# Kernel optimization log

Measured on AMD Instinct MI355X. Metric: run time of the kernel, lower is better.

Reference implementation:

```python
import jax, jax.numpy as jnp
import numpy as np

B, T, F, H, NH, L = 32, 512, 16, 64, 4, 2
HD = H // NH


def _ln(x, g, b, eps=1e-5):
    m = x.mean(-1, keepdims=True)
    v = ((x - m) ** 2).mean(-1, keepdims=True)
    return (x - m) / jnp.sqrt(v + eps) * g + b


def _glu(x, w, b):
    a, g = jnp.split(x @ w + b, 2, axis=-1)
    return a * jax.nn.sigmoid(g)


def _lstm_layer(x, w_ih, w_hh, b):
    # x: (B,T,H); PyTorch gate order i,f,g,o
    Bd = x.shape[0]

    def step(carry, xt):
        h, c = carry
        gates = xt @ w_ih + h @ w_hh + b
        i, f, g, o = jnp.split(gates, 4, axis=-1)
        c = jax.nn.sigmoid(f) * c + jax.nn.sigmoid(i) * jnp.tanh(g)
        h = jax.nn.sigmoid(o) * jnp.tanh(c)
        return (h, c), h

    z = jnp.zeros((Bd, H), x.dtype)
    _, hs = jax.lax.scan(step, (z, z), jnp.swapaxes(x, 0, 1))
    return jnp.swapaxes(hs, 0, 1)


def setup_inputs() -> dict:
    key = jax.random.key(0)
    specs = [
        ("x", (B, T, F), "n"),
        ("ip_w", (H,), "n"), ("ip_b", (H,), "n"),
        ("vsn_fc1_w", (F, H, H), "n"), ("vsn_fc1_b", (F, H), "n"),
        ("vsn_fc2_w", (F, H, 2 * H), "n"), ("vsn_fc2_b", (F, 2 * H), "n"),
        ("vsn_ln_g", (F, H), "1"), ("vsn_ln_b", (F, H), "0"),
        ("sel_fc1_w", (F * H, H), "n"), ("sel_fc1_b", (H,), "n"),
        ("sel_fc2_w", (H, 2 * F), "n"), ("sel_fc2_b", (2 * F,), "n"),
        ("sel_skip_w", (F * H, F), "n"), ("sel_skip_b", (F,), "n"),
        ("sel_ln_g", (F,), "1"), ("sel_ln_b", (F,), "0"),
        ("lstm_w_ih", (L, H, 4 * H), "n"), ("lstm_w_hh", (L, H, 4 * H), "n"), ("lstm_b", (L, 4 * H), "n"),
        ("plg_w", (H, 2 * H), "n"), ("plg_b", (2 * H,), "n"),
        ("pln_g", (H,), "1"), ("pln_b", (H,), "0"),
        ("qkv_w", (H, 3 * H), "n"), ("qkv_b", (3 * H,), "n"),
        ("ao_w", (H, H), "n"), ("ao_b", (H,), "n"),
        ("pag_w", (H, 2 * H), "n"), ("pag_b", (2 * H,), "n"),
        ("pan_g", (H,), "1"), ("pan_b", (H,), "0"),
        ("ff1_w", (H, 4 * H), "n"), ("ff1_b", (4 * H,), "n"),
        ("ff2_w", (4 * H, 2 * H), "n"), ("ff2_b", (2 * H,), "n"),
        ("ffln_g", (H,), "1"), ("ffln_b", (H,), "0"),
        ("fn_g", (H,), "1"), ("fn_b", (H,), "0"),
        ("out_w", (H, 1), "n"), ("out_b", (1,), "n"),
    ]
    keys = jax.random.split(key, len(specs))
    d = {}
    for (name, shp, kind), k in zip(specs, keys):
        if kind == "n":
            scale = 1.0 if name == "x" else 0.05
            d[name] = jax.random.normal(k, shp, jnp.float32) * scale
        elif kind == "1":
            d[name] = jnp.ones(shp, jnp.float32)
        else:
            d[name] = jnp.zeros(shp, jnp.float32)
    return d


def reference(x, ip_w, ip_b, vsn_fc1_w, vsn_fc1_b, vsn_fc2_w, vsn_fc2_b, vsn_ln_g, vsn_ln_b,
              sel_fc1_w, sel_fc1_b, sel_fc2_w, sel_fc2_b, sel_skip_w, sel_skip_b, sel_ln_g, sel_ln_b,
              lstm_w_ih, lstm_w_hh, lstm_b, plg_w, plg_b, pln_g, pln_b,
              qkv_w, qkv_b, ao_w, ao_b, pag_w, pag_b, pan_g, pan_b,
              ff1_w, ff1_b, ff2_w, ff2_b, ffln_g, ffln_b, fn_g, fn_b, out_w, out_b):
    Bd, Td, Fd = x.shape
    # input_proj: Linear(1,H) applied to each scalar feature -> (B,T,F,H)
    xp = x[..., None] * ip_w + ip_b
    # --- VSN (vectorized over B and T; torch loops over T and F) ---
    flat = xp.reshape(Bd, Td, Fd * H)
    h = jax.nn.elu(flat @ sel_fc1_w + sel_fc1_b)
    a, g = jnp.split(h @ sel_fc2_w + sel_fc2_b, 2, axis=-1)
    sel = _ln(a * jax.nn.sigmoid(g) + (flat @ sel_skip_w + sel_skip_b), sel_ln_g, sel_ln_b)
    w = jax.nn.softmax(sel, axis=-1)  # (B,T,F)
    h = jax.nn.elu(jnp.einsum('btfi,fio->btfo', xp, vsn_fc1_w) + vsn_fc1_b)
    a, g = jnp.split(jnp.einsum('btfi,fio->btfo', h, vsn_fc2_w) + vsn_fc2_b, 2, axis=-1)
    proc = _ln(a * jax.nn.sigmoid(g) + xp, vsn_ln_g, vsn_ln_b)  # (B,T,F,H)
    vsn_out = jnp.einsum('btf,btfh->bth', w, proc)
    # --- 2-layer LSTM encoder (dropout inactive in eval) ---
    seq = vsn_out
    for l in range(L):
        seq = _lstm_layer(seq, lstm_w_ih[l], lstm_w_hh[l], lstm_b[l])
    lo = _ln(_glu(seq, plg_w, plg_b) + vsn_out, pln_g, pln_b)
    # --- self-attention ---
    q, k, v = jnp.split(lo @ qkv_w + qkv_b, 3, axis=-1)
    q = q.reshape(Bd, Td, NH, HD)
    k = k.reshape(Bd, Td, NH, HD)
    v = v.reshape(Bd, Td, NH, HD)
    sc = jnp.einsum('bqhd,bkhd->bhqk', q, k) / jnp.sqrt(jnp.float32(HD))
    att = jnp.einsum('bhqk,bkhd->bqhd', jax.nn.softmax(sc, axis=-1), v).reshape(Bd, Td, H)
    att = att @ ao_w + ao_b
    at = _ln(_glu(att, pag_w, pag_b) + lo, pan_g, pan_b)
    # --- FF GRN + final norm ---
    h = jax.nn.elu(at @ ff1_w + ff1_b)
    a, g = jnp.split(h @ ff2_w + ff2_b, 2, axis=-1)
    ff = _ln(a * jax.nn.sigmoid(g) + at, ffln_g, ffln_b)
    ff = _ln(ff + at, fn_g, fn_b)
    return ff[:, -1, :] @ out_w + out_b  # (B, forecast_horizon)
```

## Files before the change

kernel.cpp:

```cpp
#include <hip/hip_runtime.h>
#include <math.h>


__device__ __forceinline__ float sigf(float x){
    return 1.f / (1.f + __expf(-x));
}
__device__ __forceinline__ float tanhf_(float x){
    float xc = fminf(fmaxf(x, -15.f), 15.f);
    float e = __expf(-2.f * xc);
    return (1.f - e) / (1.f + e);
}
__device__ __forceinline__ float eluf(float x){
    return x > 0.f ? x : (__expf(x) - 1.f);
}
__device__ __forceinline__ float wsum64(float v){
    #pragma unroll
    for (int o = 1; o < 64; o <<= 1) v += __shfl_xor(v, o, 64);
    return v;
}
__device__ __forceinline__ float wmax64(float v){
    #pragma unroll
    for (int o = 1; o < 64; o <<= 1) v = fmaxf(v, __shfl_xor(v, o, 64));
    return v;
}

#define BARRIER_LGKM() do {                                    \
    asm volatile("s_waitcnt lgkmcnt(0)" ::: "memory");         \
    __builtin_amdgcn_s_barrier();                              \
} while(0)

__global__ __launch_bounds__(256) void tft_vsn_kernel(
    const float* __restrict__ x,
    const float* __restrict__ ip_w, const float* __restrict__ ip_b,
    const float* __restrict__ vfc1w, const float* __restrict__ vfc1b,
    const float* __restrict__ vfc2w, const float* __restrict__ vfc2b,
    const float* __restrict__ vlng, const float* __restrict__ vlnb,
    const float* __restrict__ sfc1w, const float* __restrict__ sfc1b,
    const float* __restrict__ sfc2w, const float* __restrict__ sfc2b,
    const float* __restrict__ sskw, const float* __restrict__ sskb,
    const float* __restrict__ slng, const float* __restrict__ slnb,
    float* __restrict__ vsn_out)
{
    __shared__ __align__(16) float s_x[512];
    __shared__ __align__(16) float s_ipw[64];
    __shared__ __align__(16) float s_ipb[64];
    __shared__ __align__(16) float s_xp[32*65];
    __shared__ __align__(16) float s_W1[64*64];
    __shared__ __align__(16) float s_W2[64*128];
    __shared__ __align__(16) float s_Wsk[64*16];
    __shared__ __align__(16) float s_h[32*65];
    __shared__ __align__(16) float s_sel2[32*32];
    __shared__ __align__(16) float s_wsm[32*16];
    __shared__ __align__(16) float s_lng[64];
    __shared__ __align__(16) float s_lnb[64];
    __shared__ __align__(16) float s_b1[64];
    __shared__ __align__(16) float s_b2[128];

    const int tid  = threadIdx.x;
    const int pos0 = blockIdx.x * 32;
    const int m    = tid >> 3;
    const int g8   = tid & 7;
    const int j0   = g8 * 8;

    if (tid < 128) ((float4*)s_x)[tid] = *(const float4*)(x + pos0*16 + tid*4);
    if (tid < 64) { s_ipw[tid] = ip_w[tid]; s_ipb[tid] = ip_b[tid]; }
    __syncthreads();

    float accS[8];
    #pragma unroll
    for (int i = 0; i < 8; i++) accS[i] = 0.f;
    float accK0 = 0.f, accK1 = 0.f;

    for (int f = 0; f < 16; f++){
        {
            float xb = s_x[m*16 + f];
            #pragma unroll
            for (int i = 0; i < 8; i++)
                s_xp[m*65 + j0 + i] = xb * s_ipw[j0+i] + s_ipb[j0+i];
        }
        #pragma unroll
        for (int i = 0; i < 4; i++)
            ((float4*)s_W1)[tid + i*256] = *(const float4*)(sfc1w + f*4096 + (tid + i*256)*4);
        ((float4*)s_Wsk)[tid] = *(const float4*)(sskw + f*1024 + tid*4);
        __syncthreads();
        #pragma unroll 8
        for (int k = 0; k < 64; k++){
            float xv = s_xp[m*65 + k];
            const float4* wr = (const float4*)(s_W1 + k*64 + j0);
            float4 w0 = wr[0], w1 = wr[1];
            accS[0] += xv*w0.x; accS[1] += xv*w0.y; accS[2] += xv*w0.z; accS[3] += xv*w0.w;
            accS[4] += xv*w1.x; accS[5] += xv*w1.y; accS[6] += xv*w1.z; accS[7] += xv*w1.w;
            float2 wk = *(const float2*)(s_Wsk + k*16 + g8*2);
            accK0 += xv*wk.x; accK1 += xv*wk.y;
        }
        __syncthreads();
    }

    #pragma unroll
    for (int i = 0; i < 8; i++)
        s_h[m*65 + j0 + i] = eluf(accS[i] + sfc1b[j0+i]);
    ((float4*)s_W1)[tid]       = *(const float4*)(sfc2w + tid*4);
    ((float4*)s_W1)[tid + 256] = *(const float4*)(sfc2w + 1024 + tid*4);
    __syncthreads();

    {
        const int jj = g8 * 4;
        float a0 = 0.f, a1 = 0.f, a2 = 0.f, a3 = 0.f;
        #pragma unroll 8
        for (int k = 0; k < 64; k++){
            float hv = s_h[m*65 + k];
            float4 w = *(const float4*)(s_W1 + k*32 + jj);
            a0 += hv*w.x; a1 += hv*w.y; a2 += hv*w.z; a3 += hv*w.w;
        }
        s_sel2[m*32 + jj+0] = a0 + sfc2b[jj+0];
        s_sel2[m*32 + jj+1] = a1 + sfc2b[jj+1];
        s_sel2[m*32 + jj+2] = a2 + sfc2b[jj+2];
        s_sel2[m*32 + jj+3] = a3 + sfc2b[jj+3];
    }
    __syncthreads();

    {
        const int f0 = g8 * 2;
        float a0 = s_sel2[m*32 + f0],   g0 = s_sel2[m*32 + 16 + f0];
        float a1 = s_sel2[m*32 + f0+1], g1 = s_sel2[m*32 + 16 + f0+1];
        float pre0 = a0*sigf(g0) + accK0 + sskb[f0];
        float pre1 = a1*sigf(g1) + accK1 + sskb[f0+1];
        float sum = pre0 + pre1;
        sum += __shfl_xor(sum,1,8); sum += __shfl_xor(sum,2,8); sum += __shfl_xor(sum,4,8);
        float mean = sum * 0.0625f;
        float d0 = pre0 - mean, d1 = pre1 - mean;
        float vv = d0*d0 + d1*d1;
        vv += __shfl_xor(vv,1,8); vv += __shfl_xor(vv,2,8); vv += __shfl_xor(vv,4,8);
        float rstd = rsqrtf(vv * 0.0625f + 1e-5f);
        float sv0 = d0*rstd*slng[f0]   + slnb[f0];
        float sv1 = d1*rstd*slng[f0+1] + slnb[f0+1];
        float mx = fmaxf(sv0, sv1);
        mx = fmaxf(mx, __shfl_xor(mx,1,8));
        mx = fmaxf(mx, __shfl_xor(mx,2,8));
        mx = fmaxf(mx, __shfl_xor(mx,4,8));
        float e0 = __expf(sv0 - mx), e1 = __expf(sv1 - mx);
        float es = e0 + e1;
        es += __shfl_xor(es,1,8); es += __shfl_xor(es,2,8); es += __shfl_xor(es,4,8);
        float inv = 1.f / es;
        s_wsm[m*16 + f0]   = e0 * inv;
        s_wsm[m*16 + f0+1] = e1 * inv;
    }
    __syncthreads();

    float accV[8];
    #pragma unroll
    for (int i = 0; i < 8; i++) accV[i] = 0.f;

    for (int f = 0; f < 16; f++){
        {
            float xb = s_x[m*16 + f];
            #pragma unroll
            for (int i = 0; i < 8; i++)
                s_xp[m*65 + j0 + i] = xb * s_ipw[j0+i] + s_ipb[j0+i];
        }
        #pragma unroll
        for (int i = 0; i < 4; i++)
            ((float4*)s_W1)[tid + i*256] = *(const float4*)(vfc1w + f*4096 + (tid + i*256)*4);
        #pragma unroll
        for (int i = 0; i < 8; i++)
            ((float4*)s_W2)[tid + i*256] = *(const float4*)(vfc2w + f*8192 + (tid + i*256)*4);
        if (tid < 16)       ((float4*)s_b1)[tid]     = *(const float4*)(vfc1b + f*64  + tid*4);
        else if (tid < 48)  ((float4*)s_b2)[tid-16]  = *(const float4*)(vfc2b + f*128 + (tid-16)*4);
        else if (tid < 64)  ((float4*)s_lng)[tid-48] = *(const float4*)(vlng  + f*64  + (tid-48)*4);
        else if (tid < 80)  ((float4*)s_lnb)[tid-64] = *(const float4*)(vlnb  + f*64  + (tid-64)*4);
        __syncthreads();

        float ah[8];
        #pragma unroll
        for (int i = 0; i < 8; i++) ah[i] = 0.f;
        #pragma unroll 8
        for (int k = 0; k < 64; k++){
            float xv = s_xp[m*65 + k];
            const float4* wr = (const float4*)(s_W1 + k*64 + j0);
            float4 w0 = wr[0], w1 = wr[1];
            ah[0] += xv*w0.x; ah[1] += xv*w0.y; ah[2] += xv*w0.z; ah[3] += xv*w0.w;
            ah[4] += xv*w1.x; ah[5] += xv*w1.y; ah[6] += xv*w1.z; ah[7] += xv*w1.w;
        }
        #pragma unroll
        for (int i = 0; i < 8; i++)
            s_h[m*65 + j0 + i] = eluf(ah[i] + s_b1[j0+i]);
        __syncthreads();

        float aa[8], ag[8];
        #pragma unroll
        for (int i = 0; i < 8; i++){ aa[i] = 0.f; ag[i] = 0.f; }
        #pragma unroll 4
        for (int k = 0; k < 64; k++){
            float hv = s_h[m*65 + k];
            const float4* war = (const float4*)(s_W2 + k*128 + j0);
            const float4* wgr = (const float4*)(s_W2 + k*128 + 64 + j0);
            float4 wa0 = war[0], wa1 = war[1];
            float4 wg0 = wgr[0], wg1 = wgr[1];
            aa[0] += hv*wa0.x; aa[1] += hv*wa0.y; aa[2] += hv*wa0.z; aa[3] += hv*wa0.w;
            aa[4] += hv*wa1.x; aa[5] += hv*wa1.y; aa[6] += hv*wa1.z; aa[7] += hv*wa1.w;
            ag[0] += hv*wg0.x; ag[1] += hv*wg0.y; ag[2] += hv*wg0.z; ag[3] += hv*wg0.w;
            ag[4] += hv*wg1.x; ag[5] += hv*wg1.y; ag[6] += hv*wg1.z; ag[7] += hv*wg1.w;
        }
        float pre[8];
        float lsum = 0.f;
        #pragma unroll
        for (int i = 0; i < 8; i++){
            float av = aa[i] + s_b2[j0+i];
            float gv = ag[i] + s_b2[64 + j0+i];
            pre[i] = av * sigf(gv) + s_xp[m*65 + j0 + i];
            lsum += pre[i];
        }
        lsum += __shfl_xor(lsum,1,8); lsum += __shfl_xor(lsum,2,8); lsum += __shfl_xor(lsum,4,8);
        float mean = lsum * 0.015625f;
        float lvar = 0.f;
        #pragma unroll
        for (int i = 0; i < 8; i++){ float d = pre[i] - mean; lvar += d*d; }
        lvar += __shfl_xor(lvar,1,8); lvar += __shfl_xor(lvar,2,8); lvar += __shfl_xor(lvar,4,8);
        float rstd = rsqrtf(lvar * 0.015625f + 1e-5f);
        float wf = s_wsm[m*16 + f];
        #pragma unroll
        for (int i = 0; i < 8; i++)
            accV[i] += wf * ((pre[i] - mean) * rstd * s_lng[j0+i] + s_lnb[j0+i]);
        __syncthreads();
    }

    float4 o0 = make_float4(accV[0], accV[1], accV[2], accV[3]);
    float4 o1 = make_float4(accV[4], accV[5], accV[6], accV[7]);
    *(float4*)(vsn_out + (pos0 + m)*64 + j0)     = o0;
    *(float4*)(vsn_out + (pos0 + m)*64 + j0 + 4) = o1;
}

__global__ __launch_bounds__(256) void tft_xgates_kernel(
    const float* __restrict__ vsn, const float* __restrict__ w_ih,
    const float* __restrict__ bias, float* __restrict__ gpre)
{
    __shared__ __align__(16) float s_w[64*256];
    __shared__ __align__(16) float s_vT[64*20];
    __shared__ __align__(16) float s_b[256];
    const int tid  = threadIdx.x;
    const int pos0 = blockIdx.x * 16;

    #pragma unroll
    for (int i = 0; i < 16; i++)
        ((float4*)s_w)[tid + i*256] = *(const float4*)(w_ih + (tid + i*256)*4);
    s_b[tid] = bias[tid];
    {
        int mm = tid >> 4;
        int k0 = (tid & 15) * 4;
        float4 v = *(const float4*)(vsn + (pos0 + mm)*64 + k0);
        s_vT[(k0+0)*20 + mm] = v.x;
        s_vT[(k0+1)*20 + mm] = v.y;
        s_vT[(k0+2)*20 + mm] = v.z;
        s_vT[(k0+3)*20 + mm] = v.w;
    }
    __syncthreads();

    float acc[16];
    #pragma unroll
    for (int i = 0; i < 16; i++) acc[i] = 0.f;
    #pragma unroll 8
    for (int k = 0; k < 64; k++){
        float wv = s_w[k*256 + tid];
        const float4* vr = (const float4*)(s_vT + k*20);
        float4 v0 = vr[0], v1 = vr[1], v2 = vr[2], v3 = vr[3];
        acc[0]  += wv*v0.x; acc[1]  += wv*v0.y; acc[2]  += wv*v0.z; acc[3]  += wv*v0.w;
        acc[4]  += wv*v1.x; acc[5]  += wv*v1.y; acc[6]  += wv*v1.z; acc[7]  += wv*v1.w;
        acc[8]  += wv*v2.x; acc[9]  += wv*v2.y; acc[10] += wv*v2.z; acc[11] += wv*v2.w;
        acc[12] += wv*v3.x; acc[13] += wv*v3.y; acc[14] += wv*v3.z; acc[15] += wv*v3.w;
    }
    float bv = s_b[tid];
    #pragma unroll
    for (int i = 0; i < 16; i++)
        gpre[(pos0 + i)*256 + tid] = acc[i] + bv;
}

#define LDW4(P, i) make_float4((P)[(4*(i)+0)*256], (P)[(4*(i)+1)*256], \
                               (P)[(4*(i)+2)*256], (P)[(4*(i)+3)*256])

#define LSTM_CH(c) {                                                        \
    float4 h1c = h1b[c];                                                    \
    a10 += h1c.x*W1_##c.x; a11 += h1c.y*W1_##c.y;                           \
    a12 += h1c.z*W1_##c.z; a13 += h1c.w*W1_##c.w;                           \
    a20 += h1c.x*WX_##c.x; a21 += h1c.y*WX_##c.y;                           \
    a22 += h1c.z*WX_##c.z; a23 += h1c.w*WX_##c.w;                           \
    float4 h2c = h2b[c];                                                    \
    a20 += h2c.x*WH_##c.x; a21 += h2c.y*WH_##c.y;                           \
    a22 += h2c.z*WH_##c.z; a23 += h2c.w*WH_##c.w;                           \
}

__global__ __launch_bounds__(512, 1) void tft_lstm_kernel(
    const float* __restrict__ w_ih, const float* __restrict__ w_hh,
    const float* __restrict__ bias, const float* __restrict__ gpre,
    float* __restrict__ seq)
{
    __shared__ __align__(16) float s_h1[64];
    __shared__ __align__(16) float s_h2[64];
    __shared__ __align__(16) float s_g1h[512];
    __shared__ __align__(16) float s_g2h[512];
    __shared__ __align__(16) float s_gp[256];

    const int tid  = threadIdx.x;
    const int b    = blockIdx.x;
    const int g    = tid & 255;
    const int half = tid >> 8;
    const int koff = half * 32;

    const float* p1 = w_hh + koff*256 + g;
    const float* px = w_ih + 16384 + koff*256 + g;
    const float* ph = w_hh + 16384 + koff*256 + g;

    float4 W1_0 = LDW4(p1,0), W1_1 = LDW4(p1,1), W1_2 = LDW4(p1,2), W1_3 = LDW4(p1,3);
    float4 W1_4 = LDW4(p1,4), W1_5 = LDW4(p1,5), W1_6 = LDW4(p1,6), W1_7 = LDW4(p1,7);
    float4 WX_0 = LDW4(px,0), WX_1 = LDW4(px,1), WX_2 = LDW4(px,2), WX_3 = LDW4(px,3);
    float4 WX_4 = LDW4(px,4), WX_5 = LDW4(px,5), WX_6 = LDW4(px,6), WX_7 = LDW4(px,7);
    float4 WH_0 = LDW4(ph,0), WH_1 = LDW4(ph,1), WH_2 = LDW4(ph,2), WH_3 = LDW4(ph,3);
    float4 WH_4 = LDW4(ph,4), WH_5 = LDW4(ph,5), WH_6 = LDW4(ph,6), WH_7 = LDW4(ph,7);

    const float b2 = (half == 0) ? bias[256 + g] : 0.f;

    if (tid < 64) s_h1[tid] = 0.f;
    else if (tid < 128) s_h2[tid - 64] = 0.f;

    const float* gpb = gpre + (size_t)b * 512 * 256 + g;
    float gp_w = 0.f, gp_l = 0.f;
    if (half == 0){
        s_gp[g] = gpb[0];
        gp_w    = gpb[256];
        gp_l    = gpb[512];
    }
    float c1 = 0.f, c2 = 0.f;
    __syncthreads();

    const float4* h1b = (const float4*)s_h1 + half*8;
    const float4* h2b = (const float4*)s_h2 + half*8;
    float* seqb = seq + (size_t)b * 512 * 64;

    for (int n = 0; n <= 512; ++n){
        float a10 = (half == 0) ? s_gp[g] : 0.f;
        float a11 = 0.f, a12 = 0.f, a13 = 0.f;
        float a20 = b2, a21 = 0.f, a22 = 0.f, a23 = 0.f;
        LSTM_CH(0) LSTM_CH(1) LSTM_CH(2) LSTM_CH(3)
        LSTM_CH(4) LSTM_CH(5) LSTM_CH(6) LSTM_CH(7)
        float gp_n = 0.f;
        if (half == 0 && n + 3 < 512) gp_n = gpb[(n + 3) * 256];
        s_g1h[half*256 + g] = (a10 + a11) + (a12 + a13);
        s_g2h[half*256 + g] = (a20 + a21) + (a22 + a23);
        BARRIER_LGKM();

        if (tid < 64 && n < 512){
            float gi = s_g1h[tid]     + s_g1h[256+tid];
            float gf = s_g1h[64+tid]  + s_g1h[320+tid];
            float gg = s_g1h[128+tid] + s_g1h[384+tid];
            float go = s_g1h[192+tid] + s_g1h[448+tid];
            c1 = sigf(gf)*c1 + sigf(gi)*tanhf_(gg);
            s_h1[tid] = sigf(go)*tanhf_(c1);
        } else if (tid >= 64 && tid < 128 && n >= 1){
            int j = tid - 64;
            float gi = s_g2h[j]     + s_g2h[256+j];
            float gf = s_g2h[64+j]  + s_g2h[320+j];
            float gg = s_g2h[128+j] + s_g2h[384+j];
            float go = s_g2h[192+j] + s_g2h[448+j];
            c2 = sigf(gf)*c2 + sigf(gi)*tanhf_(gg);
            float h2v = sigf(go)*tanhf_(c2);
            s_h2[j] = h2v;
            seqb[(size_t)(n - 1)*64 + j] = h2v;
        }
        if (half == 0 && n + 1 < 512) s_gp[g] = gp_w;
        gp_w = gp_l; gp_l = gp_n;
        BARRIER_LGKM();
    }
}

__global__ __launch_bounds__(256) void tft_lokv_kernel(
    const float* __restrict__ seq, const float* __restrict__ vsn,
    const float* __restrict__ plgw, const float* __restrict__ plgb,
    const float* __restrict__ png,  const float* __restrict__ pnb,
    const float* __restrict__ qkvw, const float* __restrict__ qkvb,
    float* __restrict__ kbuf, float* __restrict__ vbuf,
    float* __restrict__ qlast, float* __restrict__ lolast)
{
    __shared__ __align__(16) float s_pw[64*128];
    __shared__ __align__(16) float s_qw[64*192];
    __shared__ __align__(16) float s_pb[128];
    __shared__ __align__(16) float s_png[64];
    __shared__ __align__(16) float s_pnb[64];
    __shared__ __align__(16) float s_qb[192];
    __shared__ __align__(16) float s_row[4][64];
    __shared__ __align__(16) float s_lo[4][64];

    const int tid  = threadIdx.x;
    const int lane = tid & 63;
    const int wid  = tid >> 6;

    #pragma unroll
    for (int i = 0; i < 8; i++)
        ((float4*)s_pw)[tid + i*256] = *(const float4*)(plgw + (tid + i*256)*4);
    #pragma unroll
    for (int i = 0; i < 12; i++)
        ((float4*)s_qw)[tid + i*256] = *(const float4*)(qkvw + (tid + i*256)*4);
    if (tid < 128) s_pb[tid] = plgb[tid];
    if (tid < 64){ s_png[tid] = png[tid]; s_pnb[tid] = pnb[tid]; }
    if (tid < 192) s_qb[tid] = qkvb[tid];
    __syncthreads();

    for (int it = 0; it < 16; it++){
        int mpos = blockIdx.x*64 + wid*16 + it;
        int b = mpos >> 9, t = mpos & 511;
        float sv = seq[mpos*64 + lane];
        float vs = vsn[mpos*64 + lane];
        s_row[wid][lane] = sv;
        __syncthreads();
        float a = s_pb[lane], g = s_pb[64 + lane];
        #pragma unroll 8
        for (int k = 0; k < 64; k++){
            float rv = s_row[wid][k];
            a += rv * s_pw[k*128 + lane];
            g += rv * s_pw[k*128 + 64 + lane];
        }
        float pre = a * sigf(g) + vs;
        float mean = wsum64(pre) * 0.015625f;
        float d = pre - mean;
        float vv = wsum64(d*d) * 0.015625f;
        float lo = d * rsqrtf(vv + 1e-5f) * s_png[lane] + s_pnb[lane];
        s_lo[wid][lane] = lo;
        __syncthreads();
        float ka = s_qb[64 + lane], va = s_qb[128 + lane];
        #pragma unroll 8
        for (int k = 0; k < 64; k++){
            float lv = s_lo[wid][k];
            ka += lv * s_qw[k*192 + 64 + lane];
            va += lv * s_qw[k*192 + 128 + lane];
        }
        int h = lane >> 4, dd = lane & 15;
        kbuf[((b*4 + h)*512 + t)*16 + dd] = ka;
        vbuf[((b*4 + h)*512 + t)*16 + dd] = va;
        if (t == 511){
            float qa = s_qb[lane];
            #pragma unroll 8
            for (int k = 0; k < 64; k++)
                qa += s_lo[wid][k] * s_qw[k*192 + lane];
            qlast[b*64 + lane] = qa;
            lolast[b*64 + lane] = lo;
        }
    }
}

__global__ __launch_bounds__(256) void tft_head_kernel(
    const float* __restrict__ kbuf, const float* __restrict__ vbuf,
    const float* __restrict__ qlast, const float* __restrict__ lolast,
    const float* __restrict__ aow,  const float* __restrict__ aob,
    const float* __restrict__ pagw, const float* __restrict__ pagb,
    const float* __restrict__ pang, const float* __restrict__ panb,
    const float* __restrict__ ff1w, const float* __restrict__ ff1b,
    const float* __restrict__ ff2w, const float* __restrict__ ff2b,
    const float* __restrict__ fflng, const float* __restrict__ fflnb,
    const float* __restrict__ fng,  const float* __restrict__ fnb,
    const float* __restrict__ outw, const float* __restrict__ outb,
    float* __restrict__ out)
{
    __shared__ __align__(16) float s_q[64];
    __shared__ __align__(16) float s_lo[64];
    __shared__ __align__(16) float s_sc[4*512];
    __shared__ __align__(16) float s_part[4][64];
    __shared__ __align__(16) float s_a[64];
    __shared__ __align__(16) float s_a2[64];
    __shared__ __align__(16) float s_z[128];
    __shared__ __align__(16) float s_at[64];
    __shared__ __align__(16) float s_f1[256];

    const int tid = threadIdx.x;
    const int b   = blockIdx.x;
    if (tid < 64){ s_q[tid] = qlast[b*64 + tid]; s_lo[tid] = lolast[b*64 + tid]; }
    __syncthreads();

    for (int idx = tid; idx < 2048; idx += 256){
        int h = idx >> 9, t = idx & 511;
        const float4* kr = (const float4*)(kbuf + ((b*4 + h)*512 + t)*16);
        const float4* qr = (const float4*)(s_q + h*16);
        float4 k0 = kr[0], k1 = kr[1], k2 = kr[2], k3 = kr[3];
        float4 q0 = qr[0], q1 = qr[1], q2 = qr[2], q3 = qr[3];
        float d = q0.x*k0.x + q0.y*k0.y + q0.z*k0.z + q0.w*k0.w
                + q1.x*k1.x + q1.y*k1.y + q1.z*k1.z + q1.w*k1.w
                + q2.x*k2.x + q2.y*k2.y + q2.z*k2.z + q2.w*k2.w
                + q3.x*k3.x + q3.y*k3.y + q3.z*k3.z + q3.w*k3.w;
        s_sc[idx] = d * 0.25f;
    }
    __syncthreads();
    {
        int h = tid >> 6, lane = tid & 63;
        float v[8];
        float mx = -1e30f;
        #pragma unroll
        for (int j = 0; j < 8; j++){ v[j] = s_sc[h*512 + lane + j*64]; mx = fmaxf(mx, v[j]); }
        mx = wmax64(mx);
        float sum = 0.f;
        #pragma unroll
        for (int j = 0; j < 8; j++){ v[j] = __expf(v[j] - mx); sum += v[j]; }
        sum = wsum64(sum);
        float inv = 1.f / sum;
        #pragma unroll
        for (int j = 0; j < 8; j++) s_sc[h*512 + lane + j*64] = v[j] * inv;
    }
    __syncthreads();
    {
        int j = tid & 63, part = tid >> 6;
        int h = j >> 4, dd = j & 15;
        float pa = 0.f;
        for (int t = part*128; t < (part+1)*128; t++)
            pa += s_sc[h*512 + t] * vbuf[((b*4 + h)*512 + t)*16 + dd];
        s_part[part][j] = pa;
    }
    __syncthreads();
    if (tid < 64) s_a[tid] = s_part[0][tid] + s_part[1][tid] + s_part[2][tid] + s_part[3][tid];
    __syncthreads();
    if (tid < 64){
        float o = aob[tid];
        #pragma unroll 8
        for (int k = 0; k < 64; k++) o += s_a[k] * aow[k*64 + tid];
        s_a2[tid] = o;
    }
    __syncthreads();
    if (tid < 128){
        float z = pagb[tid];
        #pragma unroll 8
        for (int k = 0; k < 64; k++) z += s_a2[k] * pagw[k*128 + tid];
        s_z[tid] = z;
    }
    __syncthreads();
    if (tid < 64){
        float pre = s_z[tid] * sigf(s_z[64 + tid]) + s_lo[tid];
        float mean = wsum64(pre) * 0.015625f;
        float d = pre - mean;
        float vv = wsum64(d*d) * 0.015625f;
        s_at[tid] = d * rsqrtf(vv + 1e-5f) * pang[tid] + panb[tid];
    }
    __syncthreads();
    {
        float hv = ff1b[tid];
        #pragma unroll 8
        for (int k = 0; k < 64; k++) hv += s_at[k] * ff1w[k*256 + tid];
        s_f1[tid] = eluf(hv);
    }
    __syncthreads();
    if (tid < 128){
        float z = ff2b[tid];
        #pragma unroll 8
        for (int k = 0; k < 256; k++) z += s_f1[k] * ff2w[k*128 + tid];
        s_z[tid] = z;
    }
    __syncthreads();
    if (tid < 64){
        float pre = s_z[tid] * sigf(s_z[64 + tid]) + s_at[tid];
        float mean = wsum64(pre) * 0.015625f;
        float d = pre - mean;
        float vv = wsum64(d*d) * 0.015625f;
        float ffv = d * rsqrtf(vv + 1e-5f) * fflng[tid] + fflnb[tid];
        float pre2 = ffv + s_at[tid];
        float mean2 = wsum64(pre2) * 0.015625f;
        float d2 = pre2 - mean2;
        float v2 = wsum64(d2*d2) * 0.015625f;
        float f2 = d2 * rsqrtf(v2 + 1e-5f) * fng[tid] + fnb[tid];
        float p = wsum64(f2 * outw[tid]);
        if (tid == 0) out[b] = p + outb[0];
    }
}

extern "C" void kernel_launch(void* const* d_in, const int* in_sizes, int n_in,
                              void* d_out, int out_size, void* d_ws, size_t ws_size,
                              hipStream_t stream)
{
    const float* x     = (const float*)d_in[0];
    const float* ip_w  = (const float*)d_in[1];
    const float* ip_b  = (const float*)d_in[2];
    const float* vfc1w = (const float*)d_in[3];
    const float* vfc1b = (const float*)d_in[4];
    const float* vfc2w = (const float*)d_in[5];
    const float* vfc2b = (const float*)d_in[6];
    const float* vlng  = (const float*)d_in[7];
    const float* vlnb  = (const float*)d_in[8];
    const float* sfc1w = (const float*)d_in[9];
    const float* sfc1b = (const float*)d_in[10];
    const float* sfc2w = (const float*)d_in[11];
    const float* sfc2b = (const float*)d_in[12];
    const float* sskw  = (const float*)d_in[13];
    const float* sskb  = (const float*)d_in[14];
    const float* slng  = (const float*)d_in[15];
    const float* slnb  = (const float*)d_in[16];
    const float* lwih  = (const float*)d_in[17];
    const float* lwhh  = (const float*)d_in[18];
    const float* lb    = (const float*)d_in[19];
    const float* plgw  = (const float*)d_in[20];
    const float* plgb  = (const float*)d_in[21];
    const float* plng  = (const float*)d_in[22];
    const float* plnb  = (const float*)d_in[23];
    const float* qkvw  = (const float*)d_in[24];
    const float* qkvb  = (const float*)d_in[25];
    const float* aow   = (const float*)d_in[26];
    const float* aob   = (const float*)d_in[27];
    const float* pagw  = (const float*)d_in[28];
    const float* pagb  = (const float*)d_in[29];
    const float* pang  = (const float*)d_in[30];
    const float* panb  = (const float*)d_in[31];
    const float* ff1w  = (const float*)d_in[32];
    const float* ff1b  = (const float*)d_in[33];
    const float* ff2w  = (const float*)d_in[34];
    const float* ff2b  = (const float*)d_in[35];
    const float* fflng = (const float*)d_in[36];
    const float* fflnb = (const float*)d_in[37];
    const float* fng   = (const float*)d_in[38];
    const float* fnb   = (const float*)d_in[39];
    const float* outw  = (const float*)d_in[40];
    const float* outb  = (const float*)d_in[41];

    float* ws      = (float*)d_ws;
    float* vsn_out = ws;
    float* seq     = ws + 1048576;
    float* gpre    = ws + 2*1048576;
    float* kbuf    = ws + 6*1048576;
    float* vbuf    = ws + 7*1048576;
    float* qlast   = ws + 8*1048576;
    float* lolast  = qlast + 2048;
    float* outp    = (float*)d_out;

    tft_vsn_kernel<<<512, 256, 0, stream>>>(x, ip_w, ip_b, vfc1w, vfc1b, vfc2w, vfc2b,
                                            vlng, vlnb, sfc1w, sfc1b, sfc2w, sfc2b,
                                            sskw, sskb, slng, slnb, vsn_out);
    tft_xgates_kernel<<<1024, 256, 0, stream>>>(vsn_out, lwih, lb, gpre);
    tft_lstm_kernel<<<32, 512, 0, stream>>>(lwih, lwhh, lb, gpre, seq);
    tft_lokv_kernel<<<256, 256, 0, stream>>>(seq, vsn_out, plgw, plgb, plng, plnb,
                                             qkvw, qkvb, kbuf, vbuf, qlast, lolast);
    tft_head_kernel<<<32, 256, 0, stream>>>(kbuf, vbuf, qlast, lolast, aow, aob,
                                            pagw, pagb, pang, panb, ff1w, ff1b,
                                            ff2w, ff2b, fflng, fflnb, fng, fnb,
                                            outw, outb, outp);
}
```

Measured before the change: 767.9 us.

## Restructure LSTM recurrence to reduce gates in-wave and use one barrier per step

Reorganizes the persistent 2-layer LSTM kernel so each wave owns 16 hidden units. Lanes split the K dimension and gate pairs, and gate partial sums are combined with cross-lane shuffles instead of being staged in shared memory. Hidden states are double-buffered, which removes one of the two block barriers per timestep and the serial 64-thread gate phase. The cost is more weight registers for layer-2 waves (which take the full K=128 concat) and redundant activation math across lanes.

```diff
diff --git a/kernel.cpp b/kernel.cpp
--- a/kernel.cpp
+++ b/kernel.cpp
@@ -274,100 +274,133 @@
         gpre[(pos0 + i)*256 + tid] = acc[i] + bv;
 }
 
-#define LDW4(P, i) make_float4((P)[(4*(i)+0)*256], (P)[(4*(i)+1)*256], \
-                               (P)[(4*(i)+2)*256], (P)[(4*(i)+3)*256])
-
-#define LSTM_CH(c) {                                                        \
-    float4 h1c = h1b[c];                                                    \
-    a10 += h1c.x*W1_##c.x; a11 += h1c.y*W1_##c.y;                           \
-    a12 += h1c.z*W1_##c.z; a13 += h1c.w*W1_##c.w;                           \
-    a20 += h1c.x*WX_##c.x; a21 += h1c.y*WX_##c.y;                           \
-    a22 += h1c.z*WX_##c.z; a23 += h1c.w*WX_##c.w;                           \
-    float4 h2c = h2b[c];                                                    \
-    a20 += h2c.x*WH_##c.x; a21 += h2c.y*WH_##c.y;                           \
-    a22 += h2c.z*WH_##c.z; a23 += h2c.w*WH_##c.w;                           \
-}
+#define LW(P, c) make_float4((P)[(4*(c)+0)*256], (P)[(4*(c)+1)*256], \
+                             (P)[(4*(c)+2)*256], (P)[(4*(c)+3)*256])
+
+#define ACC(c, hv) { float4 h_ = (hv);                                      \
+    a0  += h_.x*WA_##c.x; a0x += h_.y*WA_##c.y;                             \
+    a0  += h_.z*WA_##c.z; a0x += h_.w*WA_##c.w;                             \
+    a1  += h_.x*WB_##c.x; a1x += h_.y*WB_##c.y;                             \
+    a1  += h_.z*WB_##c.z; a1x += h_.w*WB_##c.w; }
 
 __global__ __launch_bounds__(512, 1) void tft_lstm_kernel(
     const float* __restrict__ w_ih, const float* __restrict__ w_hh,
     const float* __restrict__ bias, const float* __restrict__ gpre,
     float* __restrict__ seq)
 {
-    __shared__ __align__(16) float s_h1[64];
-    __shared__ __align__(16) float s_h2[64];
-    __shared__ __align__(16) float s_g1h[512];
-    __shared__ __align__(16) float s_g2h[512];
-    __shared__ __align__(16) float s_gp[256];
-
-    const int tid  = threadIdx.x;
-    const int b    = blockIdx.x;
-    const int g    = tid & 255;
-    const int half = tid >> 8;
-    const int koff = half * 32;
-
-    const float* p1 = w_hh + koff*256 + g;
-    const float* px = w_ih + 16384 + koff*256 + g;
-    const float* ph = w_hh + 16384 + koff*256 + g;
-
-    float4 W1_0 = LDW4(p1,0), W1_1 = LDW4(p1,1), W1_2 = LDW4(p1,2), W1_3 = LDW4(p1,3);
-    float4 W1_4 = LDW4(p1,4), W1_5 = LDW4(p1,5), W1_6 = LDW4(p1,6), W1_7 = LDW4(p1,7);
-    float4 WX_0 = LDW4(px,0), WX_1 = LDW4(px,1), WX_2 = LDW4(px,2), WX_3 = LDW4(px,3);
-    float4 WX_4 = LDW4(px,4), WX_5 = LDW4(px,5), WX_6 = LDW4(px,6), WX_7 = LDW4(px,7);
-    float4 WH_0 = LDW4(ph,0), WH_1 = LDW4(ph,1), WH_2 = LDW4(ph,2), WH_3 = LDW4(ph,3);
-    float4 WH_4 = LDW4(ph,4), WH_5 = LDW4(ph,5), WH_6 = LDW4(ph,6), WH_7 = LDW4(ph,7);
-
-    const float b2 = (half == 0) ? bias[256 + g] : 0.f;
-
-    if (tid < 64) s_h1[tid] = 0.f;
-    else if (tid < 128) s_h2[tid - 64] = 0.f;
-
-    const float* gpb = gpre + (size_t)b * 512 * 256 + g;
-    float gp_w = 0.f, gp_l = 0.f;
-    if (half == 0){
-        s_gp[g] = gpb[0];
-        gp_w    = gpb[256];
-        gp_l    = gpb[512];
-    }
-    float c1 = 0.f, c2 = 0.f;
-    __syncthreads();
-
-    const float4* h1b = (const float4*)s_h1 + half*8;
-    const float4* h2b = (const float4*)s_h2 + half*8;
+    __shared__ __align__(16) float s_h1[2][64];
+    __shared__ __align__(16) float s_h2[2][64];
+
+    const int tid   = threadIdx.x;
+    const int b     = blockIdx.x;
+    const int lane  = tid & 63;
+    const int wid   = tid >> 6;
+    const int role  = wid >> 2;
+    const int j     = ((wid & 3) << 4) | (lane & 15);
+    const int kh    = (lane >> 4) & 1;
+    const int gpair = (lane >> 5) & 1;
+    const bool sub0 = (lane & 48) == 0;
+
+    const int g0 = (gpair ? 64 : 0) + j;
+    const int g1 = (gpair ? 192 : 128) + j;
+
+    const float* bA;
+    const float* bB;
+    if (role == 0){
+        bA = w_hh + (kh * 32) * 256 + g0;
+        bB = w_hh + (kh * 32) * 256 + g1;
+    } else {
+        const float* mat = kh ? (w_hh + 16384) : (w_ih + 16384);
+        bA = mat + g0;
+        bB = mat + g1;
+    }
+    const float4 z4 = make_float4(0.f, 0.f, 0.f, 0.f);
+    float4 WA_0 = LW(bA,0), WA_1 = LW(bA,1), WA_2 = LW(bA,2), WA_3 = LW(bA,3);
+    float4 WA_4 = LW(bA,4), WA_5 = LW(bA,5), WA_6 = LW(bA,6), WA_7 = LW(bA,7);
+    float4 WB_0 = LW(bB,0), WB_1 = LW(bB,1), WB_2 = LW(bB,2), WB_3 = LW(bB,3);
+    float4 WB_4 = LW(bB,4), WB_5 = LW(bB,5), WB_6 = LW(bB,6), WB_7 = LW(bB,7);
+    float4 WA_8 = z4, WA_9 = z4, WA_10 = z4, WA_11 = z4;
+    float4 WA_12 = z4, WA_13 = z4, WA_14 = z4, WA_15 = z4;
+    float4 WB_8 = z4, WB_9 = z4, WB_10 = z4, WB_11 = z4;
+    float4 WB_12 = z4, WB_13 = z4, WB_14 = z4, WB_15 = z4;
+    if (role == 1){
+        WA_8  = LW(bA,8);  WA_9  = LW(bA,9);  WA_10 = LW(bA,10); WA_11 = LW(bA,11);
+        WA_12 = LW(bA,12); WA_13 = LW(bA,13); WA_14 = LW(bA,14); WA_15 = LW(bA,15);
+        WB_8  = LW(bB,8);  WB_9  = LW(bB,9);  WB_10 = LW(bB,10); WB_11 = LW(bB,11);
+        WB_12 = LW(bB,12); WB_13 = LW(bB,13); WB_14 = LW(bB,14); WB_15 = LW(bB,15);
+    }
+
+    const float b2A = (role == 1 && kh == 0) ? bias[256 + g0] : 0.f;
+    const float b2B = (role == 1 && kh == 0) ? bias[256 + g1] : 0.f;
+
+    const bool gpl = (role == 0 && kh == 0);
+    const float* gpbA = gpre + (size_t)b * 131072 + g0;
+    const float* gpbB = gpre + (size_t)b * 131072 + g1;
+    float gA0 = 0.f, gA1 = 0.f, gA2 = 0.f;
+    float gB0 = 0.f, gB1 = 0.f, gB2 = 0.f;
+    if (gpl){
+        gA0 = gpbA[0];   gB0 = gpbB[0];
+        gA1 = gpbA[256]; gB1 = gpbB[256];
+        gA2 = gpbA[512]; gB2 = gpbB[512];
+    }
+
+    if (tid < 64){ s_h1[0][tid] = 0.f; s_h1[1][tid] = 0.f; }
+    else if (tid < 128){ s_h2[0][tid-64] = 0.f; s_h2[1][tid-64] = 0.f; }
+    float c_ = 0.f;
+    __syncthreads();
+
+    float* rd1 = &s_h1[1][0]; float* wr1 = &s_h1[0][0];
+    float* rd2 = &s_h2[1][0]; float* wr2 = &s_h2[0][0];
     float* seqb = seq + (size_t)b * 512 * 64;
 
     for (int n = 0; n <= 512; ++n){
-        float a10 = (half == 0) ? s_gp[g] : 0.f;
-        float a11 = 0.f, a12 = 0.f, a13 = 0.f;
-        float a20 = b2, a21 = 0.f, a22 = 0.f, a23 = 0.f;
-        LSTM_CH(0) LSTM_CH(1) LSTM_CH(2) LSTM_CH(3)
-        LSTM_CH(4) LSTM_CH(5) LSTM_CH(6) LSTM_CH(7)
-        float gp_n = 0.f;
-        if (half == 0 && n + 3 < 512) gp_n = gpb[(n + 3) * 256];
-        s_g1h[half*256 + g] = (a10 + a11) + (a12 + a13);
-        s_g2h[half*256 + g] = (a20 + a21) + (a22 + a23);
+        float a0  = (role == 0) ? gA0 : b2A;
+        float a1  = (role == 0) ? gB0 : b2B;
+        float a0x = 0.f, a1x = 0.f;
+        if (role == 0){
+            const float4* hp = (const float4*)rd1 + kh * 8;
+            ACC(0, hp[0]) ACC(1, hp[1]) ACC(2, hp[2]) ACC(3, hp[3])
+            ACC(4, hp[4]) ACC(5, hp[5]) ACC(6, hp[6]) ACC(7, hp[7])
+        } else {
+            const float4* hp = (const float4*)(kh ? rd2 : rd1);
+            ACC(0, hp[0])  ACC(1, hp[1])  ACC(2, hp[2])  ACC(3, hp[3])
+            ACC(4, hp[4])  ACC(5, hp[5])  ACC(6, hp[6])  ACC(7, hp[7])
+            ACC(8, hp[8])  ACC(9, hp[9])  ACC(10,hp[10]) ACC(11,hp[11])
+            ACC(12,hp[12]) ACC(13,hp[13]) ACC(14,hp[14]) ACC(15,hp[15])
+        }
+        float A0 = a0 + a0x;
+        float A1 = a1 + a1x;
+        A0 += __shfl_xor(A0, 16, 64);
+        A1 += __shfl_xor(A1, 16, 64);
+        float B0 = __shfl_xor(A0, 32, 64);
+        float B1 = __shfl_xor(A1, 32, 64);
+        float gi = gpair ? B0 : A0;
+        float gf = gpair ? A0 : B0;
+        float gg = gpair ? B1 : A1;
+        float go = gpair ? A1 : B1;
+
+        if (role == 0){
+            if (n < 512){
+                c_ = sigf(gf)*c_ + sigf(gi)*tanhf_(gg);
+                float h1v = sigf(go)*tanhf_(c_);
+                if (sub0) wr1[j] = h1v;
+            }
+            if (gpl){
+                gA0 = gA1; gA1 = gA2;
+                gB0 = gB1; gB1 = gB2;
+                if (n + 3 < 512){ gA2 = gpbA[(n+3)*256]; gB2 = gpbB[(n+3)*256]; }
+            }
+        } else if (n >= 1){
+            c_ = sigf(gf)*c_ + sigf(gi)*tanhf_(gg);
+            float h2v = sigf(go)*tanhf_(c_);
+            if (sub0){
+                wr2[j] = h2v;
+                seqb[(size_t)(n-1)*64 + j] = h2v;
+            }
+        }
         BARRIER_LGKM();
-
-        if (tid < 64 && n < 512){
-            float gi = s_g1h[tid]     + s_g1h[256+tid];
-            float gf = s_g1h[64+tid]  + s_g1h[320+tid];
-            float gg = s_g1h[128+tid] + s_g1h[384+tid];
-            float go = s_g1h[192+tid] + s_g1h[448+tid];
-            c1 = sigf(gf)*c1 + sigf(gi)*tanhf_(gg);
-            s_h1[tid] = sigf(go)*tanhf_(c1);
-        } else if (tid >= 64 && tid < 128 && n >= 1){
-            int j = tid - 64;
-            float gi = s_g2h[j]     + s_g2h[256+j];
-            float gf = s_g2h[64+j]  + s_g2h[320+j];
-            float gg = s_g2h[128+j] + s_g2h[384+j];
-            float go = s_g2h[192+j] + s_g2h[448+j];
-            c2 = sigf(gf)*c2 + sigf(gi)*tanhf_(gg);
-            float h2v = sigf(go)*tanhf_(c2);
-            s_h2[j] = h2v;
-            seqb[(size_t)(n - 1)*64 + j] = h2v;
-        }
-        if (half == 0 && n + 1 < 512) s_gp[g] = gp_w;
-        gp_w = gp_l; gp_l = gp_n;
-        BARRIER_LGKM();
+        float* t1 = rd1; rd1 = wr1; wr1 = t1;
+        float* t2 = rd2; rd2 = wr2; wr2 = t2;
     }
 }
 
```

New measurement: 794.2 us. 1.03x slower.

## Split LSTM recurrence across 1024 threads with per-layer warps and shuffle reduction

Applied to the files above, without the earlier changes.

The wavefront-pipelined 2-layer LSTM kernel grows from 512 to 1024 threads. Warps 0-7 now compute layer-1 gates and warps 8-15 compute layer-2 gates, with each wave's two 32-lane halves holding half of the K reduction in registers and combining it through a cross-lane shuffle. This removes the half-block shared-memory partial sums and the shared gpre staging buffer, which shortens the per-timestep critical path. In exchange it adds a divergent branch on layer, uses more waves per block, and puts more warps into each of the two barriers per timestep.

```diff
diff --git a/kernel.cpp b/kernel.cpp
--- a/kernel.cpp
+++ b/kernel.cpp
@@ -274,99 +274,101 @@
         gpre[(pos0 + i)*256 + tid] = acc[i] + bv;
 }
 
-#define LDW4(P, i) make_float4((P)[(4*(i)+0)*256], (P)[(4*(i)+1)*256], \
-                               (P)[(4*(i)+2)*256], (P)[(4*(i)+3)*256])
-
-#define LSTM_CH(c) {                                                        \
-    float4 h1c = h1b[c];                                                    \
-    a10 += h1c.x*W1_##c.x; a11 += h1c.y*W1_##c.y;                           \
-    a12 += h1c.z*W1_##c.z; a13 += h1c.w*W1_##c.w;                           \
-    a20 += h1c.x*WX_##c.x; a21 += h1c.y*WX_##c.y;                           \
-    a22 += h1c.z*WX_##c.z; a23 += h1c.w*WX_##c.w;                           \
-    float4 h2c = h2b[c];                                                    \
-    a20 += h2c.x*WH_##c.x; a21 += h2c.y*WH_##c.y;                           \
-    a22 += h2c.z*WH_##c.z; a23 += h2c.w*WH_##c.w;                           \
-}
-
-__global__ __launch_bounds__(512, 1) void tft_lstm_kernel(
+#define LWR(P, c) make_float4((P)[(4*(c)+0)*256], (P)[(4*(c)+1)*256], \
+                              (P)[(4*(c)+2)*256], (P)[(4*(c)+3)*256])
+
+#define ACCW(c, hv) { float4 h_ = (hv);                                     \
+    a0 += h_.x*W_##c.x; a1 += h_.y*W_##c.y;                                 \
+    a2 += h_.z*W_##c.z; a3 += h_.w*W_##c.w; }
+
+__global__ __launch_bounds__(1024, 1) void tft_lstm_kernel(
     const float* __restrict__ w_ih, const float* __restrict__ w_hh,
     const float* __restrict__ bias, const float* __restrict__ gpre,
     float* __restrict__ seq)
 {
     __shared__ __align__(16) float s_h1[64];
     __shared__ __align__(16) float s_h2[64];
-    __shared__ __align__(16) float s_g1h[512];
-    __shared__ __align__(16) float s_g2h[512];
-    __shared__ __align__(16) float s_gp[256];
+    __shared__ __align__(16) float s_g1[256];
+    __shared__ __align__(16) float s_g2[256];
 
     const int tid  = threadIdx.x;
     const int b    = blockIdx.x;
-    const int g    = tid & 255;
-    const int half = tid >> 8;
-    const int koff = half * 32;
-
-    const float* p1 = w_hh + koff*256 + g;
-    const float* px = w_ih + 16384 + koff*256 + g;
-    const float* ph = w_hh + 16384 + koff*256 + g;
-
-    float4 W1_0 = LDW4(p1,0), W1_1 = LDW4(p1,1), W1_2 = LDW4(p1,2), W1_3 = LDW4(p1,3);
-    float4 W1_4 = LDW4(p1,4), W1_5 = LDW4(p1,5), W1_6 = LDW4(p1,6), W1_7 = LDW4(p1,7);
-    float4 WX_0 = LDW4(px,0), WX_1 = LDW4(px,1), WX_2 = LDW4(px,2), WX_3 = LDW4(px,3);
-    float4 WX_4 = LDW4(px,4), WX_5 = LDW4(px,5), WX_6 = LDW4(px,6), WX_7 = LDW4(px,7);
-    float4 WH_0 = LDW4(ph,0), WH_1 = LDW4(ph,1), WH_2 = LDW4(ph,2), WH_3 = LDW4(ph,3);
-    float4 WH_4 = LDW4(ph,4), WH_5 = LDW4(ph,5), WH_6 = LDW4(ph,6), WH_7 = LDW4(ph,7);
-
-    const float b2 = (half == 0) ? bias[256 + g] : 0.f;
+    const int lane = tid & 63;
+    const int wid  = tid >> 6;
+    const bool isL2 = (wid >= 8);
+    const int gate = ((wid & 7) << 5) | (lane & 31);
+    const int part = lane >> 5;
+
+    const float* wp;
+    if (!isL2) wp = w_hh + part * 32 * 256 + gate;
+    else       wp = (part ? (w_hh + 16384) : (w_ih + 16384)) + gate;
+
+    const float4 z4 = make_float4(0.f, 0.f, 0.f, 0.f);
+    float4 W_0 = LWR(wp,0), W_1 = LWR(wp,1), W_2 = LWR(wp,2), W_3 = LWR(wp,3);
+    float4 W_4 = LWR(wp,4), W_5 = LWR(wp,5), W_6 = LWR(wp,6), W_7 = LWR(wp,7);
+    float4 W_8 = z4, W_9 = z4, W_10 = z4, W_11 = z4;
+    float4 W_12 = z4, W_13 = z4, W_14 = z4, W_15 = z4;
+    if (isL2){
+        W_8  = LWR(wp,8);  W_9  = LWR(wp,9);  W_10 = LWR(wp,10); W_11 = LWR(wp,11);
+        W_12 = LWR(wp,12); W_13 = LWR(wp,13); W_14 = LWR(wp,14); W_15 = LWR(wp,15);
+    }
+
+    const float b2 = (isL2 && part == 0) ? bias[256 + gate] : 0.f;
+    const bool gpl = (!isL2 && part == 0);
+    const float* gpb = gpre + (size_t)b * 131072 + gate;
+    float gq0 = 0.f, gq1 = 0.f, gq2 = 0.f;
+    if (gpl){ gq0 = gpb[0]; gq1 = gpb[256]; gq2 = gpb[512]; }
 
     if (tid < 64) s_h1[tid] = 0.f;
     else if (tid < 128) s_h2[tid - 64] = 0.f;
-
-    const float* gpb = gpre + (size_t)b * 512 * 256 + g;
-    float gp_w = 0.f, gp_l = 0.f;
-    if (half == 0){
-        s_gp[g] = gpb[0];
-        gp_w    = gpb[256];
-        gp_l    = gpb[512];
-    }
-    float c1 = 0.f, c2 = 0.f;
-    __syncthreads();
-
-    const float4* h1b = (const float4*)s_h1 + half*8;
-    const float4* h2b = (const float4*)s_h2 + half*8;
+    float c_ = 0.f;
+    __syncthreads();
+
     float* seqb = seq + (size_t)b * 512 * 64;
 
     for (int n = 0; n <= 512; ++n){
-        float a10 = (half == 0) ? s_gp[g] : 0.f;
-        float a11 = 0.f, a12 = 0.f, a13 = 0.f;
-        float a20 = b2, a21 = 0.f, a22 = 0.f, a23 = 0.f;
-        LSTM_CH(0) LSTM_CH(1) LSTM_CH(2) LSTM_CH(3)
-        LSTM_CH(4) LSTM_CH(5) LSTM_CH(6) LSTM_CH(7)
-        float gp_n = 0.f;
-        if (half == 0 && n + 3 < 512) gp_n = gpb[(n + 3) * 256];
-        s_g1h[half*256 + g] = (a10 + a11) + (a12 + a13);
-        s_g2h[half*256 + g] = (a20 + a21) + (a22 + a23);
+        float a0 = isL2 ? b2 : gq0;
+        float a1 = 0.f, a2 = 0.f, a3 = 0.f;
+        if (!isL2){
+            const float4* hp = (const float4*)s_h1 + part * 8;
+            ACCW(0, hp[0]) ACCW(1, hp[1]) ACCW(2, hp[2]) ACCW(3, hp[3])
+            ACCW(4, hp[4]) ACCW(5, hp[5]) ACCW(6, hp[6]) ACCW(7, hp[7])
+        } else {
+            const float4* hp = (const float4*)(part ? s_h2 : s_h1);
+            ACCW(0, hp[0])  ACCW(1, hp[1])  ACCW(2, hp[2])  ACCW(3, hp[3])
+            ACCW(4, hp[4])  ACCW(5, hp[5])  ACCW(6, hp[6])  ACCW(7, hp[7])
+            ACCW(8, hp[8])  ACCW(9, hp[9])  ACCW(10,hp[10]) ACCW(11,hp[11])
+            ACCW(12,hp[12]) ACCW(13,hp[13]) ACCW(14,hp[14]) ACCW(15,hp[15])
+        }
+        float A = (a0 + a1) + (a2 + a3);
+        A += __shfl_xor(A, 32, 64);
+        if (lane < 32){
+            if (!isL2) s_g1[gate] = A;
+            else       s_g2[gate] = A;
+        }
+        if (gpl){
+            gq0 = gq1; gq1 = gq2;
+            if (n + 3 < 512) gq2 = gpb[(n + 3) * 256];
+        }
         BARRIER_LGKM();
 
-        if (tid < 64 && n < 512){
-            float gi = s_g1h[tid]     + s_g1h[256+tid];
-            float gf = s_g1h[64+tid]  + s_g1h[320+tid];
-            float gg = s_g1h[128+tid] + s_g1h[384+tid];
-            float go = s_g1h[192+tid] + s_g1h[448+tid];
-            c1 = sigf(gf)*c1 + sigf(gi)*tanhf_(gg);
-            s_h1[tid] = sigf(go)*tanhf_(c1);
-        } else if (tid >= 64 && tid < 128 && n >= 1){
-            int j = tid - 64;
-            float gi = s_g2h[j]     + s_g2h[256+j];
-            float gf = s_g2h[64+j]  + s_g2h[320+j];
-            float gg = s_g2h[128+j] + s_g2h[384+j];
-            float go = s_g2h[192+j] + s_g2h[448+j];
-            c2 = sigf(gf)*c2 + sigf(gi)*tanhf_(gg);
-            float h2v = sigf(go)*tanhf_(c2);
-            s_h2[j] = h2v;
-            seqb[(size_t)(n - 1)*64 + j] = h2v;
-        }
-        if (half == 0 && n + 1 < 512) s_gp[g] = gp_w;
-        gp_w = gp_l; gp_l = gp_n;
+        if (wid == 0){
+            if (n < 512){
+                float gi = s_g1[lane],     gf = s_g1[64+lane],
+                      gg = s_g1[128+lane], go = s_g1[192+lane];
+                c_ = sigf(gf)*c_ + sigf(gi)*tanhf_(gg);
+                s_h1[lane] = sigf(go)*tanhf_(c_);
+            }
+        } else if (wid == 1){
+            if (n >= 1){
+                float gi = s_g2[lane],     gf = s_g2[64+lane],
+                      gg = s_g2[128+lane], go = s_g2[192+lane];
+                c_ = sigf(gf)*c_ + sigf(gi)*tanhf_(gg);
+                float h2v = sigf(go)*tanhf_(c_);
+                s_h2[lane] = h2v;
+                seqb[(size_t)(n-1)*64 + lane] = h2v;
+            }
+        }
         BARRIER_LGKM();
     }
 }
@@ -626,7 +628,7 @@
                                             vlng, vlnb, sfc1w, sfc1b, sfc2w, sfc2b,
                                             sskw, sskb, slng, slnb, vsn_out);
     tft_xgates_kernel<<<1024, 256, 0, stream>>>(vsn_out, lwih, lb, gpre);
-    tft_lstm_kernel<<<32, 512, 0, stream>>>(lwih, lwhh, lb, gpre, seq);
+    tft_lstm_kernel<<<32, 1024, 0, stream>>>(lwih, lwhh, lb, gpre, seq);
     tft_lokv_kernel<<<256, 256, 0, stream>>>(seq, vsn_out, plgw, plgb, plng, plnb,
                                              qkvw, qkvb, kbuf, vbuf, qlast, lolast);
     tft_head_kernel<<<32, 256, 0, stream>>>(kbuf, vbuf, qlast, lolast, aow, aob,
```

Measured after the change: 1.067 ms. 39.0% more time.
